# Optimization experiments

Measured on AMD Instinct MI355X. Metric: run time of the kernel, lower is better.

The kernel has to match this reference:

```python
import jax, jax.numpy as jnp
import numpy as np

DT = 0.001
TAU_INV = 1.0 / 0.006   # tau_mem_inv == tau_syn_inv for both cells
V_TH = 1.0              # norse defaults: v_leak=0, v_reset=0


def heaviside(x):
    return (x > 0).astype(x.dtype)


def setup_inputs() -> dict:
    key = jax.random.key(0)
    k1, k2, k3 = jax.random.split(key, 3)
    T, B, I, H, O = 128, 2048, 64, 256, 16
    inp = jax.random.normal(k1, (T, B, I), dtype=jnp.float32)
    # torch.nn.Linear default init ~ U(-1/sqrt(fan_in), 1/sqrt(fan_in))
    w1 = jax.random.uniform(k2, (H, I), jnp.float32, -1.0, 1.0) / np.sqrt(I)
    w2 = jax.random.uniform(k3, (O, H), jnp.float32, -1.0, 1.0) / np.sqrt(H)
    return {"input": inp, "w1": w1, "w2": w2}


def _snn_forward(inp, w1, w2):
    B = inp.shape[1]
    H, O = w1.shape[0], w2.shape[0]
    decay = 1.0 - DT * TAU_INV

    def step(carry, x_t):
        v1, i1, v2, i2 = carry
        # LIF cell (hidden layer)
        g1 = x_t @ w1.T                              # [B, H]
        v_dec = v1 + DT * TAU_INV * (i1 - v1)        # Euler membrane update
        i_dec = i1 * decay                           # synaptic decay
        z = heaviside(v_dec - V_TH)                  # spikes
        v1n = (1.0 - z) * v_dec                      # reset to 0 where spiked
        i1n = i_dec + g1
        # LI cell (readout)
        g2 = z @ w2.T                                # [B, O]
        v2n = v2 + DT * TAU_INV * (i2 - v2)
        i2n = i2 * decay + g2
        return (v1n, i1n, v2n, i2n), (z, v2n)

    init = (jnp.zeros((B, H), inp.dtype), jnp.zeros((B, H), inp.dtype),
            jnp.zeros((B, O), inp.dtype), jnp.zeros((B, O), inp.dtype))
    _, (zs, ys) = jax.lax.scan(step, init, inp)
    score = jnp.max(ys, axis=0)                      # amax over time -> [B, O]
    spikes_mean = jnp.mean(jnp.sum(zs, axis=(0, 2)))
    return score, spikes_mean


def reference(input, w1, w2):
    return _snn_forward(input, w1, w2)
```

## Files before the change

kernel.cpp:

```cpp
#include <hip/hip_runtime.h>

#define T_STEPS 128
#define BATCH   2048
#define IN_F    64
#define HID     256
#define OUT_F   16
#define CH      8
#define TROWS   16
#define HHALF   128
#define NCHUNK  (T_STEPS / CH)
#define SLAB    (BATCH * OUT_F)

typedef __attribute__((ext_vector_type(8))) short bf16x8;
typedef __attribute__((ext_vector_type(4))) float f32x4;
typedef unsigned short u16;
typedef unsigned int   u32;

__device__ __forceinline__ u16 f2bf(float f) {
    u32 u = __float_as_uint(f);
    u += 0x7fffu + ((u >> 16) & 1u);
    return (u16)(u >> 16);
}
__device__ __forceinline__ float bf2f(u16 h) {
    return __uint_as_float(((u32)h) << 16);
}
__device__ __forceinline__ bf16x8 pack8(float4 a, float4 b) {
    bf16x8 r;
    r[0] = (short)f2bf(a.x); r[1] = (short)f2bf(a.y);
    r[2] = (short)f2bf(a.z); r[3] = (short)f2bf(a.w);
    r[4] = (short)f2bf(b.x); r[5] = (short)f2bf(b.y);
    r[6] = (short)f2bf(b.z); r[7] = (short)f2bf(b.w);
    return r;
}

__global__ void snn_init_kernel(float* __restrict__ out) {
    if (threadIdx.x == 0 && blockIdx.x == 0) out[BATCH * OUT_F] = 0.0f;
}

__global__ void __launch_bounds__(512, 2)
snn_l1_kernel(const float* __restrict__ x, const float* __restrict__ w1,
              const float* __restrict__ w2, u16* __restrict__ g2p,
              float* __restrict__ out)
{
    const int tid  = threadIdx.x;
    const int lane = tid & 63;
    const int wv   = tid >> 6;
    const int hi   = lane >> 4;
    const int l15  = lane & 15;
    const int tile = blockIdx.x & 127;
    const int half = blockIdx.x >> 7;
    const int row0 = tile * TROWS;

    __shared__ __attribute__((aligned(16))) u16 xl[CH * TROWS * IN_F];
    __shared__ __attribute__((aligned(16))) u16 zb[CH * TROWS * HHALF];
    __shared__ float sacc;
    if (tid == 0) sacc = 0.f;

    const f32x4 zf = {0.f, 0.f, 0.f, 0.f};
    const float dt_tau = (float)(0.001 * (1.0 / 0.006));
    const float decay  = (float)(1.0 - 0.001 * (1.0 / 0.006));

    const int hcol = half * HHALF + wv * 16 + l15;
    bf16x8 w1f[2];
#pragma unroll
    for (int kt = 0; kt < 2; ++kt)
        w1f[kt] = pack8(*(const float4*)&w1[hcol * IN_F + kt * 32 + hi * 8],
                        *(const float4*)&w1[hcol * IN_F + kt * 32 + hi * 8 + 4]);

    bf16x8 w2f[4];
#pragma unroll
    for (int kt = 0; kt < 4; ++kt) {
        const int k0 = half * HHALF + kt * 32 + hi * 8;
        w2f[kt] = pack8(*(const float4*)&w2[l15 * HID + k0],
                        *(const float4*)&w2[l15 * HID + k0 + 4]);
    }

    int wofs[2];
    const float* gp[2];
    const size_t cstride = (size_t)CH * BATCH * IN_F;
#pragma unroll
    for (int j = 0; j < 2; ++j) {
        const int v  = tid + 512 * j;
        const int vs = v >> 7;
        const int vr = (v >> 3) & 15;
        const int vk = (v & 7) * 8;
        wofs[j] = (vs * TROWS + vr) * IN_F + (vk ^ ((vr & 7) << 3));
        gp[j]   = x + ((size_t)vs * BATCH + row0 + vr) * IN_F + vk;
    }
    float4 ra[2], rb[2];
#pragma unroll
    for (int j = 0; j < 2; ++j) {
        ra[j] = *(const float4*)gp[j];
        rb[j] = *(const float4*)(gp[j] + 4);
        *(bf16x8*)&xl[wofs[j]] = pack8(ra[j], rb[j]);
    }
#pragma unroll
    for (int j = 0; j < 2; ++j) {
        ra[j] = *(const float4*)(gp[j] + cstride);
        rb[j] = *(const float4*)(gp[j] + cstride + 4);
    }

    f32x4 v1 = zf, i1 = zf;
    float scnt = 0.f;
    const int xswz = (l15 & 7) << 3;
    int zoff[4];
#pragma unroll
    for (int r = 0; r < 4; ++r) {
        const int zr = 4 * hi + r;
        zoff[r] = zr * HHALF + ((wv * 16 + l15) ^ ((zr & 15) << 3));
    }
    __syncthreads();

    for (int c = 0; c < NCHUNK; ++c) {
        f32x4 g1[CH];
#pragma unroll
        for (int s = 0; s < CH; ++s) {
            const u16* xrow = &xl[(s * TROWS + l15) * IN_F];
            const bf16x8 xf0 = *(const bf16x8*)(xrow + ((hi * 8) ^ xswz));
            const bf16x8 xf1 = *(const bf16x8*)(xrow + ((32 + hi * 8) ^ xswz));
            g1[s] = __builtin_amdgcn_mfma_f32_16x16x32_bf16(xf0, w1f[0], zf, 0, 0, 0);
            g1[s] = __builtin_amdgcn_mfma_f32_16x16x32_bf16(xf1, w1f[1], g1[s], 0, 0, 0);
        }

#pragma unroll
        for (int s = 0; s < CH; ++s) {
            u16* zw = &zb[s * TROWS * HHALF];
#pragma unroll
            for (int r = 0; r < 4; ++r) {
                const float vd = fmaf(dt_tau, i1[r] - v1[r], v1[r]);
                const float id = i1[r] * decay;
                const bool  sp = vd > 1.0f;
                v1[r] = sp ? 0.f : vd;
                i1[r] = id + g1[s][r];
                scnt += sp ? 1.f : 0.f;
                zw[zoff[r]] = sp ? (u16)0x3F80 : (u16)0;
            }
        }

        __syncthreads();

        if (c + 1 < NCHUNK) {
#pragma unroll
            for (int j = 0; j < 2; ++j)
                *(bf16x8*)&xl[wofs[j]] = pack8(ra[j], rb[j]);
            if (c + 2 < NCHUNK) {
#pragma unroll
                for (int j = 0; j < 2; ++j) {
                    const float* g = gp[j] + 2 * cstride;
                    ra[j] = *(const float4*)g;
                    rb[j] = *(const float4*)(g + 4);
                    gp[j] += cstride;
                }
            }
        }

        {
            const u16* zr2 = &zb[(wv * TROWS + l15) * HHALF];
            const int rsw = l15 << 3;
            const bf16x8 z0 = *(const bf16x8*)(zr2 + ((0 * 32 + hi * 8) ^ rsw));
            const bf16x8 z1 = *(const bf16x8*)(zr2 + ((1 * 32 + hi * 8) ^ rsw));
            const bf16x8 z2 = *(const bf16x8*)(zr2 + ((2 * 32 + hi * 8) ^ rsw));
            const bf16x8 z3 = *(const bf16x8*)(zr2 + ((3 * 32 + hi * 8) ^ rsw));
            f32x4 ga = __builtin_amdgcn_mfma_f32_16x16x32_bf16(z0, w2f[0], zf, 0, 0, 0);
            f32x4 gb = __builtin_amdgcn_mfma_f32_16x16x32_bf16(z1, w2f[1], zf, 0, 0, 0);
            ga = __builtin_amdgcn_mfma_f32_16x16x32_bf16(z2, w2f[2], ga, 0, 0, 0);
            gb = __builtin_amdgcn_mfma_f32_16x16x32_bf16(z3, w2f[3], gb, 0, 0, 0);
            const f32x4 g2 = ga + gb;
            u16* dst = g2p + (size_t)half * (T_STEPS * SLAB)
                     + (size_t)(c * CH + wv) * SLAB + (row0 + 4 * hi) * OUT_F + l15;
#pragma unroll
            for (int r = 0; r < 4; ++r) dst[r * OUT_F] = f2bf(g2[r]);
        }

        __syncthreads();
    }

#pragma unroll
    for (int m = 1; m < 64; m <<= 1) scnt += __shfl_xor(scnt, m, 64);
    if (lane == 0) atomicAdd(&sacc, scnt);
    __syncthreads();
    if (tid == 0) atomicAdd(&out[BATCH * OUT_F], sacc * (1.0f / BATCH));
}

__global__ void __launch_bounds__(128)
snn_li_kernel(const u16* __restrict__ g2p, float* __restrict__ out)
{
    const int gid = blockIdx.x * 128 + threadIdx.x;
    const u16* p0 = g2p + gid;
    const u16* p1 = g2p + (size_t)T_STEPS * SLAB + gid;
    const float dt_tau = (float)(0.001 * (1.0 / 0.006));
    const float decay  = (float)(1.0 - 0.001 * (1.0 / 0.006));
    float v2 = 0.f, i2 = 0.f, ymax = -1e30f;
#pragma unroll 8
    for (int t = 0; t < T_STEPS; ++t) {
        const float g = bf2f(p0[(size_t)t * SLAB]) + bf2f(p1[(size_t)t * SLAB]);
        v2 = fmaf(dt_tau, i2 - v2, v2);
        ymax = fmaxf(ymax, v2);
        i2 = i2 * decay + g;
    }
    out[gid] = ymax;
}

extern "C" void kernel_launch(void* const* d_in, const int* in_sizes, int n_in,
                              void* d_out, int out_size, void* d_ws, size_t ws_size,
                              hipStream_t stream) {
    const float* x  = (const float*)d_in[0];
    const float* w1 = (const float*)d_in[1];
    const float* w2 = (const float*)d_in[2];
    float* out = (float*)d_out;
    u16* g2p = (u16*)d_ws;

    hipLaunchKernelGGL(snn_init_kernel, dim3(1), dim3(64), 0, stream, out);
    hipLaunchKernelGGL(snn_l1_kernel, dim3(256), dim3(512), 0, stream,
                       x, w1, w2, g2p, out);
    hipLaunchKernelGGL(snn_li_kernel, dim3(BATCH * OUT_F / 128), dim3(128), 0,
                       stream, g2p, out);
}
```

Baseline: 55.39 us.

## Double timestep chunk size, count spikes via wave ballot, use library bf16 convert

```diff
diff --git a/kernel.cpp b/kernel.cpp
--- a/kernel.cpp
+++ b/kernel.cpp
@@ -1,11 +1,12 @@
 #include <hip/hip_runtime.h>
+#include <hip/hip_bf16.h>
 
 #define T_STEPS 128
 #define BATCH   2048
 #define IN_F    64
 #define HID     256
 #define OUT_F   16
-#define CH      8
+#define CH      16
 #define TROWS   16
 #define HHALF   128
 #define NCHUNK  (T_STEPS / CH)
@@ -17,9 +18,9 @@
 typedef unsigned int   u32;
 
 __device__ __forceinline__ u16 f2bf(float f) {
-    u32 u = __float_as_uint(f);
-    u += 0x7fffu + ((u >> 16) & 1u);
-    return (u16)(u >> 16);
+    union { __hip_bfloat16 h; u16 u; } cv;
+    cv.h = __float2bfloat16(f);
+    return cv.u;
 }
 __device__ __forceinline__ float bf2f(u16 h) {
     return __uint_as_float(((u32)h) << 16);
@@ -75,11 +76,11 @@
                         *(const float4*)&w2[l15 * HID + k0 + 4]);
     }
 
-    int wofs[2];
-    const float* gp[2];
+    int wofs[4];
+    const float* gp[4];
     const size_t cstride = (size_t)CH * BATCH * IN_F;
 #pragma unroll
-    for (int j = 0; j < 2; ++j) {
+    for (int j = 0; j < 4; ++j) {
         const int v  = tid + 512 * j;
         const int vs = v >> 7;
         const int vr = (v >> 3) & 15;
@@ -87,21 +88,21 @@
         wofs[j] = (vs * TROWS + vr) * IN_F + (vk ^ ((vr & 7) << 3));
         gp[j]   = x + ((size_t)vs * BATCH + row0 + vr) * IN_F + vk;
     }
-    float4 ra[2], rb[2];
-#pragma unroll
-    for (int j = 0; j < 2; ++j) {
+    float4 ra[4], rb[4];
+#pragma unroll
+    for (int j = 0; j < 4; ++j) {
         ra[j] = *(const float4*)gp[j];
         rb[j] = *(const float4*)(gp[j] + 4);
         *(bf16x8*)&xl[wofs[j]] = pack8(ra[j], rb[j]);
     }
 #pragma unroll
-    for (int j = 0; j < 2; ++j) {
+    for (int j = 0; j < 4; ++j) {
         ra[j] = *(const float4*)(gp[j] + cstride);
         rb[j] = *(const float4*)(gp[j] + cstride + 4);
     }
 
     f32x4 v1 = zf, i1 = zf;
-    float scnt = 0.f;
+    int wcnt = 0;
     const int xswz = (l15 & 7) << 3;
     int zoff[4];
 #pragma unroll
@@ -125,27 +126,27 @@
 #pragma unroll
         for (int s = 0; s < CH; ++s) {
             u16* zw = &zb[s * TROWS * HHALF];
+            const f32x4 vd = v1 + dt_tau * (i1 - v1);
+            const f32x4 id = i1 * decay;
 #pragma unroll
             for (int r = 0; r < 4; ++r) {
-                const float vd = fmaf(dt_tau, i1[r] - v1[r], v1[r]);
-                const float id = i1[r] * decay;
-                const bool  sp = vd > 1.0f;
-                v1[r] = sp ? 0.f : vd;
-                i1[r] = id + g1[s][r];
-                scnt += sp ? 1.f : 0.f;
+                const bool sp = vd[r] > 1.0f;
+                v1[r] = sp ? 0.f : vd[r];
+                wcnt += __popcll(__ballot(sp));
                 zw[zoff[r]] = sp ? (u16)0x3F80 : (u16)0;
             }
+            i1 = id + g1[s];
         }
 
         __syncthreads();
 
         if (c + 1 < NCHUNK) {
 #pragma unroll
-            for (int j = 0; j < 2; ++j)
+            for (int j = 0; j < 4; ++j)
                 *(bf16x8*)&xl[wofs[j]] = pack8(ra[j], rb[j]);
             if (c + 2 < NCHUNK) {
 #pragma unroll
-                for (int j = 0; j < 2; ++j) {
+                for (int j = 0; j < 4; ++j) {
                     const float* g = gp[j] + 2 * cstride;
                     ra[j] = *(const float4*)g;
                     rb[j] = *(const float4*)(g + 4);
@@ -154,8 +155,10 @@
             }
         }
 
-        {
-            const u16* zr2 = &zb[(wv * TROWS + l15) * HHALF];
+#pragma unroll
+        for (int ss = 0; ss < 2; ++ss) {
+            const int s = ss * 8 + wv;
+            const u16* zr2 = &zb[(s * TROWS + l15) * HHALF];
             const int rsw = l15 << 3;
             const bf16x8 z0 = *(const bf16x8*)(zr2 + ((0 * 32 + hi * 8) ^ rsw));
             const bf16x8 z1 = *(const bf16x8*)(zr2 + ((1 * 32 + hi * 8) ^ rsw));
@@ -167,7 +170,7 @@
             gb = __builtin_amdgcn_mfma_f32_16x16x32_bf16(z3, w2f[3], gb, 0, 0, 0);
             const f32x4 g2 = ga + gb;
             u16* dst = g2p + (size_t)half * (T_STEPS * SLAB)
-                     + (size_t)(c * CH + wv) * SLAB + (row0 + 4 * hi) * OUT_F + l15;
+                     + (size_t)(c * CH + s) * SLAB + (row0 + 4 * hi) * OUT_F + l15;
 #pragma unroll
             for (int r = 0; r < 4; ++r) dst[r * OUT_F] = f2bf(g2[r]);
         }
@@ -175,9 +178,7 @@
         __syncthreads();
     }
 
-#pragma unroll
-    for (int m = 1; m < 64; m <<= 1) scnt += __shfl_xor(scnt, m, 64);
-    if (lane == 0) atomicAdd(&sacc, scnt);
+    if (lane == 0) atomicAdd(&sacc, (float)wcnt);
     __syncthreads();
     if (tid == 0) atomicAdd(&out[BATCH * OUT_F], sacc * (1.0f / BATCH));
 }
```

Measured after the change: 55.45 us. No clear change (+0.1%).
